# Performance work log

Measured on AMD Instinct MI355X. Metric: run time of the kernel, lower is better.

The kernel has to match this reference:

```python
import jax, jax.numpy as jnp
import numpy as np

L, BT, D = 1024, 64, 768
HID, NH, K = 192, 4, 5
T = 16
Hh = Ww = 32  # H = W = sqrt(L)


def setup_inputs() -> dict:
    key = jax.random.key(0)
    ks = jax.random.split(key, 10)
    s = 0.02
    def w(i, shape):
        return jax.random.normal(ks[i], shape, jnp.float32) * s
    return {
        "x": jax.random.normal(ks[0], (L, BT, D), jnp.float32),
        "fc1_w": w(1, (HID, D)), "fc1_b": jnp.zeros((HID,), jnp.float32),
        "convA_w": w(2, (64, HID)), "convA_b": jnp.zeros((64,), jnp.float32),
        "convB_w": w(3, (HID, 64)), "convB_b": jnp.zeros((HID,), jnp.float32),
        "ln_g": jnp.ones((HID,), jnp.float32), "ln_b": jnp.zeros((HID,), jnp.float32),
        "qkv_w": w(4, (3 * HID, HID)), "qkv_b": jnp.zeros((3 * HID,), jnp.float32),
        "rpb": w(5, (NH, 2 * K - 1, 2 * K - 1)),
        "proj_w": w(6, (HID, HID)), "proj_b": jnp.zeros((HID,), jnp.float32),
        "fc2_w": w(7, (D, HID)), "fc2_b": jnp.zeros((D,), jnp.float32),
    }


def _layernorm(x, g, b, eps=1e-5):
    # fp32 LayerNorm over last dim (matches the fp16-safe LayerNorm subclass)
    xf = x.astype(jnp.float32)
    m = xf.mean(-1, keepdims=True)
    v = ((xf - m) ** 2).mean(-1, keepdims=True)
    return ((xf - m) / jnp.sqrt(v + eps) * g + b).astype(x.dtype)


def _natten2d(x, qkv_w, qkv_b, rpb, proj_w, proj_b):
    # Neighborhood attention: each pixel attends to an edge-clamped KxK window.
    B, H, W, C = x.shape
    hd = C // NH
    qkv = (x @ qkv_w.T + qkv_b).reshape(B, H, W, 3, NH, hd)
    q, k, v = qkv[..., 0, :, :], qkv[..., 1, :, :], qkv[..., 2, :, :]
    q = q * (hd ** -0.5)
    half = K // 2
    ih = jnp.clip(jnp.arange(H) - half, 0, H - K)[:, None] + jnp.arange(K)  # [H,K]
    iw = jnp.clip(jnp.arange(W) - half, 0, W - K)[:, None] + jnp.arange(K)  # [W,K]
    k_nb = k[:, ih][:, :, :, iw]  # [B,H,K,W,K,NH,hd]
    v_nb = v[:, ih][:, :, :, iw]
    attn = jnp.einsum('bijnd,bixjynd->bnijxy', q, k_nb)  # [B,NH,H,W,K,K]
    bh = ih - jnp.arange(H)[:, None] + (K - 1)  # [H,K] in [0, 2K-2]
    bw = iw - jnp.arange(W)[:, None] + (K - 1)  # [W,K]
    bias = rpb[:, bh][:, :, :, bw]              # [NH,H,K,W,K]
    attn = attn + bias.transpose(0, 1, 3, 2, 4)[None]
    a = jax.nn.softmax(attn.reshape(B, NH, H, W, K * K), axis=-1)
    a = a.reshape(B, NH, H, W, K, K)
    out = jnp.einsum('bnijxy,bixjynd->bijnd', a, v_nb).reshape(B, H, W, C)
    return out @ proj_w.T + proj_b


def _forward(x, fc1_w, fc1_b, convA_w, convA_b, convB_w, convB_b,
             ln_g, ln_b, qkv_w, qkv_b, rpb, proj_w, proj_b, fc2_w, fc2_b):
    # x: [L, BT, D]
    xs = x @ fc1_w.T + fc1_b  # [L, BT, HID]
    # 1x1 Conv1d pair over the channel (HID) dim; dropout is identity in eval
    a = jnp.einsum('lbc,oc->lbo', xs, convA_w) + convA_b
    b_ = jnp.einsum('lbo,co->lbc', a, convB_w) + convB_b
    xs = b_ + xs  # scale = 1
    xs = jax.nn.gelu(xs, approximate=False)
    xs = xs.transpose(1, 0, 2).reshape(BT, Hh, Ww, HID)  # [BT,H,W,C]
    xs = xs + _natten2d(_layernorm(xs, ln_g, ln_b), qkv_w, qkv_b, rpb, proj_w, proj_b)
    xs = xs.reshape(BT, L, HID).transpose(1, 0, 2)  # [L,BT,HID]
    xs = xs @ fc2_w.T + fc2_b  # [L,BT,D]
    x = x + xs
    x = x.transpose(1, 0, 2).reshape(BT, Hh, Ww, D)
    x = x.reshape(BT // T, T, Hh, Ww, D).transpose(0, 4, 1, 2, 3)  # [B,D,T,H,W]
    return x


def reference(x, fc1_w, fc1_b, convA_w, convA_b, convB_w, convB_b,
              ln_g, ln_b, qkv_w, qkv_b, rpb, proj_w, proj_b, fc2_w, fc2_b):
    return _forward(x, fc1_w, fc1_b, convA_w, convA_b, convB_w, convB_b,
                    ln_g, ln_b, qkv_w, qkv_b, rpb, proj_w, proj_b, fc2_w, fc2_b)
```

## Files before the change

### kernel.cpp

```cpp
#include <hip/hip_runtime.h>
#include <hip/hip_bf16.h>
#include <math.h>


typedef __attribute__((ext_vector_type(4))) float f32x4;
typedef __attribute__((ext_vector_type(8))) __bf16 bf16x8;
typedef const __attribute__((address_space(1))) void gv_t;
typedef __attribute__((address_space(3))) void lv_t;

__device__ __forceinline__ uint2 pack_bf16x4(float4 v) {
  union { unsigned short u[4]; uint2 d; } o;
  __hip_bfloat16 b0 = __float2bfloat16(v.x);
  __hip_bfloat16 b1 = __float2bfloat16(v.y);
  __hip_bfloat16 b2 = __float2bfloat16(v.z);
  __hip_bfloat16 b3 = __float2bfloat16(v.w);
  o.u[0] = *(unsigned short*)&b0; o.u[1] = *(unsigned short*)&b1;
  o.u[2] = *(unsigned short*)&b2; o.u[3] = *(unsigned short*)&b3;
  return o.d;
}

__global__ __launch_bounds__(512, 4) void fc1_kernel(
    const float* __restrict__ X, const __hip_bfloat16* __restrict__ W,
    const float* __restrict__ bias, __hip_bfloat16* __restrict__ C) {
  __shared__ __hip_bfloat16 Asm[2][128 * 64];
  __shared__ __hip_bfloat16 Bsm[2][192 * 64];

  const int tid = threadIdx.x;
  const int lane = tid & 63;
  const int wave = tid >> 6;
  const int lid = blockIdx.x;
  const int bm0 = (((lid & 7) << 6) + (lid >> 3)) << 7;
  const int wm0 = (wave >> 1) * 32;
  const int wn0 = (wave & 1) * 96;
  const int l15 = lane & 15;
  const int l7 = lane & 7;
  const int lg = lane >> 4;

  f32x4 acc[2][6] = {};
  float4 ar[4];

  auto stageB = [&](int buf, int k0) {
#pragma unroll
    for (int it = 0; it < 3; ++it) {
      int ci = tid + it * 512;
      int r = ci >> 3, c = ci & 7;
      int sc = c ^ (r & 7);
      const __hip_bfloat16* src = W + (size_t)r * 768 + k0 + sc * 8;
      __builtin_amdgcn_global_load_lds((gv_t*)src, (lv_t*)&Bsm[buf][ci * 8], 16, 0, 0);
    }
  };
  auto loadA = [&](int k0) {
#pragma unroll
    for (int q = 0; q < 2; ++q) {
      int ci = tid + q * 512;
      int r = ci >> 3, c = ci & 7;
      int sc = c ^ (r & 7);
      const float* src = X + (size_t)(bm0 + r) * 768 + k0 + sc * 8;
      ar[2 * q] = *(const float4*)src;
      ar[2 * q + 1] = *(const float4*)(src + 4);
    }
  };
  auto writeA = [&](int buf) {
#pragma unroll
    for (int q = 0; q < 2; ++q) {
      int ci = tid + q * 512;
      uint2 a = pack_bf16x4(ar[2 * q]);
      uint2 b = pack_bf16x4(ar[2 * q + 1]);
      uint4 w; w.x = a.x; w.y = a.y; w.z = b.x; w.w = b.y;
      *(uint4*)&Asm[buf][ci * 8] = w;
    }
  };

  stageB(0, 0);
  loadA(0);
  int cur = 0;
  for (int kt = 0; kt < 12; ++kt) {
    writeA(cur);
    __syncthreads();
    if (kt < 11) { stageB(cur ^ 1, (kt + 1) * 64); loadA((kt + 1) * 64); }
    const char* Ab = (const char*)&Asm[cur][0];
    const char* Bb = (const char*)&Bsm[cur][0];
#pragma unroll
    for (int kk = 0; kk < 2; ++kk) {
      const int ks = (lg * 16 + kk * 64) ^ (l7 << 4);
      bf16x8 af[2], bfr[6];
#pragma unroll
      for (int mi = 0; mi < 2; ++mi)
        af[mi] = *(const bf16x8*)(Ab + (wm0 + mi * 16 + l15) * 128 + ks);
#pragma unroll
      for (int nj = 0; nj < 6; ++nj)
        bfr[nj] = *(const bf16x8*)(Bb + (wn0 + nj * 16 + l15) * 128 + ks);
#pragma unroll
      for (int mi = 0; mi < 2; ++mi)
#pragma unroll
        for (int nj = 0; nj < 6; ++nj)
          acc[mi][nj] = __builtin_amdgcn_mfma_f32_16x16x32_bf16(
              af[mi], bfr[nj], acc[mi][nj], 0, 0, 0);
    }
    cur ^= 1;
  }

#pragma unroll
  for (int nj = 0; nj < 6; ++nj) {
    const int n = wn0 + nj * 16 + l15;
    const float bi = bias[n];
#pragma unroll
    for (int mi = 0; mi < 2; ++mi) {
      const int mb = bm0 + wm0 + mi * 16 + lg * 4;
#pragma unroll
      for (int r = 0; r < 4; ++r)
        C[(size_t)(mb + r) * 192 + n] = __float2bfloat16(acc[mi][nj][r] + bi);
    }
  }
}

template <int MODE>
__global__ __launch_bounds__(256) void gemm_fullk_kernel(
    const __hip_bfloat16* __restrict__ A, const __hip_bfloat16* __restrict__ W,
    const float* __restrict__ bias, const __hip_bfloat16* __restrict__ res,
    const float* __restrict__ xin, void* __restrict__ Cout, int N) {
  __shared__ __hip_bfloat16 Asm[3 * 128 * 64];
  __shared__ __hip_bfloat16 Bsm[3 * 64 * 64];

  const int tid = threadIdx.x;
  const int lane = tid & 63;
  const int wave = tid >> 6;

  const int gx = gridDim.x;
  const int lid = blockIdx.y * gx + blockIdx.x;
  const int seq = lid >> 3;
  const int bm0 = (((lid & 7) << 6) + seq / gx) << 7;
  const int bn0 = (seq % gx) * 64;

  const int wm0 = (wave >> 1) * 64;
  const int wn0 = (wave & 1) * 32;
  const int l15 = lane & 15;
  const int l7 = lane & 7;
  const int lg = lane >> 4;

#pragma unroll
  for (int it = 0; it < 12; ++it) {
    int ci = tid + it * 256;
    int sec = ci >> 10, ri = ci & 1023;
    int r = ri >> 3, c = ri & 7;
    int sc = c ^ (r & 7);
    const __hip_bfloat16* src = A + (size_t)(bm0 + r) * 192 + sec * 64 + sc * 8;
    __builtin_amdgcn_global_load_lds((gv_t*)src, (lv_t*)&Asm[ci * 8], 16, 0, 0);
  }
#pragma unroll
  for (int it = 0; it < 6; ++it) {
    int ci = tid + it * 256;
    int sec = ci >> 9, ri = ci & 511;
    int r = ri >> 3, c = ri & 7;
    int sc = c ^ (r & 7);
    const __hip_bfloat16* src = W + (size_t)(bn0 + r) * 192 + sec * 64 + sc * 8;
    __builtin_amdgcn_global_load_lds((gv_t*)src, (lv_t*)&Bsm[ci * 8], 16, 0, 0);
  }
  __syncthreads();

  f32x4 acc[4][2] = {};
  const char* Ab = (const char*)Asm;
  const char* Bb = (const char*)Bsm;
#pragma unroll
  for (int kk = 0; kk < 6; ++kk) {
    const int sec = kk >> 1, k2 = kk & 1;
    const int ks = (lg * 16 + k2 * 64) ^ (l7 << 4);
    bf16x8 af[4], bfr[2];
#pragma unroll
    for (int mi = 0; mi < 4; ++mi)
      af[mi] = *(const bf16x8*)(Ab + sec * 16384 + (wm0 + mi * 16 + l15) * 128 + ks);
#pragma unroll
    for (int nj = 0; nj < 2; ++nj)
      bfr[nj] = *(const bf16x8*)(Bb + sec * 8192 + (wn0 + nj * 16 + l15) * 128 + ks);
#pragma unroll
    for (int mi = 0; mi < 4; ++mi)
#pragma unroll
      for (int nj = 0; nj < 2; ++nj) {
        if constexpr (MODE == 2)
          acc[mi][nj] = __builtin_amdgcn_mfma_f32_16x16x32_bf16(
              bfr[nj], af[mi], acc[mi][nj], 0, 0, 0);
        else
          acc[mi][nj] = __builtin_amdgcn_mfma_f32_16x16x32_bf16(
              af[mi], bfr[nj], acc[mi][nj], 0, 0, 0);
      }
  }

  if constexpr (MODE == 2) {
    float* Cf = (float*)Cout;
#pragma unroll
    for (int nj = 0; nj < 2; ++nj) {
      const int n0 = bn0 + wn0 + nj * 16 + lg * 4;
      const f32x4 bi4 = *(const f32x4*)(bias + n0);
#pragma unroll
      for (int mi = 0; mi < 4; ++mi) {
        const int m = bm0 + wm0 + mi * 16 + l15;
        const int b = m >> 10;
        const int ll = m & 1023;
        const f32x4 xv = *(const f32x4*)(xin + (size_t)((ll << 6) | b) * 768 + n0);
        const size_t ob = (((size_t)(b >> 4) * 768 + n0) * 16 + (b & 15)) * 1024 + ll;
#pragma unroll
        for (int r = 0; r < 4; ++r)
          Cf[ob + (size_t)r * 16384] = acc[mi][nj][r] + bi4[r] + xv[r];
      }
    }
  } else {
    __hip_bfloat16* Cb = (__hip_bfloat16*)Cout;
#pragma unroll
    for (int nj = 0; nj < 2; ++nj) {
      const int n = bn0 + wn0 + nj * 16 + l15;
      const float bi = bias[n];
#pragma unroll
      for (int mi = 0; mi < 4; ++mi) {
        const int mb = bm0 + wm0 + mi * 16 + lg * 4;
        f32x4 v = acc[mi][nj];
#pragma unroll
        for (int r = 0; r < 4; ++r) {
          const int m = mb + r;
          float val = v[r] + bi;
          if constexpr (MODE == 1) val += __bfloat162float(res[(size_t)m * N + n]);
          Cb[(size_t)m * N + n] = __float2bfloat16(val);
        }
      }
    }
  }
}

__global__ __launch_bounds__(256) void cvt_weights_kernel(
    const float* __restrict__ s0, const float* __restrict__ s1,
    const float* __restrict__ s2, const float* __restrict__ s3,
    const float* __restrict__ s4, const float* __restrict__ s5,
    __hip_bfloat16* __restrict__ d0, __hip_bfloat16* __restrict__ d1,
    __hip_bfloat16* __restrict__ d2, __hip_bfloat16* __restrict__ d3,
    __hip_bfloat16* __restrict__ d4, __hip_bfloat16* __restrict__ d5) {
  int i = blockIdx.x * 256 + threadIdx.x;
  const float* src; __hip_bfloat16* dst; int off;
  if      (i < 36864)  { src = s0; dst = d0; off = i; }
  else if (i < 39936)  { src = s1; dst = d1; off = i - 36864; }
  else if (i < 43008)  { src = s2; dst = d2; off = i - 39936; }
  else if (i < 70656)  { src = s3; dst = d3; off = i - 43008; }
  else if (i < 79872)  { src = s4; dst = d4; off = i - 70656; }
  else                 { src = s5; dst = d5; off = i - 79872; }
  ((uint2*)dst)[off] = pack_bf16x4(((const float4*)src)[off]);
}

__global__ __launch_bounds__(256, 2) void bottleneck_kernel(
    const __hip_bfloat16* __restrict__ xs0,
    const __hip_bfloat16* __restrict__ wA, const float* __restrict__ bA,
    const __hip_bfloat16* __restrict__ wB, const float* __restrict__ bB,
    const float* __restrict__ ln_g, const float* __restrict__ ln_b,
    __hip_bfloat16* __restrict__ xs_sp, __hip_bfloat16* __restrict__ ln_sp) {
  __shared__ __hip_bfloat16 xt[3 * 64 * 64];
  __shared__ __hip_bfloat16 wAs[3 * 64 * 64];
  __shared__ __hip_bfloat16 wBs[192 * 64];
  __shared__ __hip_bfloat16 a2[64 * 64];

  const int tid = threadIdx.x;
  const int lane = tid & 63;
  const int wave = tid >> 6;
  const int bm0 = blockIdx.x * 64;
  const int l15 = lane & 15;
  const int lg = lane >> 4;
  const int wm0 = (wave >> 1) * 32;

#pragma unroll
  for (int it = 0; it < 6; ++it) {
    int ci = tid + it * 256;
    int sec = ci >> 9, ri = ci & 511;
    int r = ri >> 3, c = ri & 7;
    int sc = c ^ (r & 7);
    const __hip_bfloat16* src = xs0 + (size_t)(bm0 + r) * 192 + sec * 64 + sc * 8;
    __builtin_amdgcn_global_load_lds((gv_t*)src, (lv_t*)&xt[ci * 8], 16, 0, 0);
  }
#pragma unroll
  for (int it = 0; it < 6; ++it) {
    int ci = tid + it * 256;
    int sec = ci >> 9, ri = ci & 511;
    int r = ri >> 3, c = ri & 7;
    int sc = c ^ (r & 7);
    const __hip_bfloat16* src = wA + (size_t)r * 192 + sec * 64 + sc * 8;
    __builtin_amdgcn_global_load_lds((gv_t*)src, (lv_t*)&wAs[ci * 8], 16, 0, 0);
  }
#pragma unroll
  for (int it = 0; it < 6; ++it) {
    int ci = tid + it * 256;
    int r = ci >> 3, c = ci & 7;
    int sc = c ^ (r & 7);
    const __hip_bfloat16* src = wB + (size_t)r * 64 + sc * 8;
    __builtin_amdgcn_global_load_lds((gv_t*)src, (lv_t*)&wBs[ci * 8], 16, 0, 0);
  }
  __syncthreads();

  {
    const int wn0 = (wave & 1) * 32;
    f32x4 acc1[2][2] = {};
    const char* Ab = (const char*)xt;
    const char* Bb = (const char*)wAs;
#pragma unroll
    for (int kk = 0; kk < 6; ++kk) {
      const int sec = kk >> 1, k2 = kk & 1;
      const int ks = (lg * 16 + k2 * 64) ^ ((l15 & 7) << 4);
      bf16x8 af[2], bfr[2];
#pragma unroll
      for (int mi = 0; mi < 2; ++mi)
        af[mi] = *(const bf16x8*)(Ab + sec * 8192 + (wm0 + mi * 16 + l15) * 128 + ks);
#pragma unroll
      for (int nj = 0; nj < 2; ++nj)
        bfr[nj] = *(const bf16x8*)(Bb + sec * 8192 + (wn0 + nj * 16 + l15) * 128 + ks);
#pragma unroll
      for (int mi = 0; mi < 2; ++mi)
#pragma unroll
        for (int nj = 0; nj < 2; ++nj)
          acc1[mi][nj] = __builtin_amdgcn_mfma_f32_16x16x32_bf16(
              af[mi], bfr[nj], acc1[mi][nj], 0, 0, 0);
    }
#pragma unroll
    for (int nj = 0; nj < 2; ++nj) {
      const int n = wn0 + nj * 16 + l15;
      const float bi = bA[n];
#pragma unroll
      for (int mi = 0; mi < 2; ++mi)
#pragma unroll
        for (int r = 0; r < 4; ++r) {
          const int row = wm0 + mi * 16 + lg * 4 + r;
          a2[row * 64 + (((n >> 3) ^ (row & 7)) << 3) + (n & 7)] =
              __float2bfloat16(acc1[mi][nj][r] + bi);
        }
    }
  }
  __syncthreads();

  const int wn0 = (wave & 1) * 96;
  f32x4 acc2[2][6] = {};
  {
    const char* Ab = (const char*)a2;
    const char* Bb = (const char*)wBs;
#pragma unroll
    for (int kk = 0; kk < 2; ++kk) {
      const int ks = (lg * 16 + kk * 64) ^ ((l15 & 7) << 4);
      bf16x8 af[2], bfr[6];
#pragma unroll
      for (int mi = 0; mi < 2; ++mi)
        af[mi] = *(const bf16x8*)(Ab + (wm0 + mi * 16 + l15) * 128 + ks);
#pragma unroll
      for (int nj = 0; nj < 6; ++nj)
        bfr[nj] = *(const bf16x8*)(Bb + (wn0 + nj * 16 + l15) * 128 + ks);
#pragma unroll
      for (int mi = 0; mi < 2; ++mi)
#pragma unroll
        for (int nj = 0; nj < 6; ++nj)
          acc2[mi][nj] = __builtin_amdgcn_mfma_f32_16x16x32_bf16(
              af[mi], bfr[nj], acc2[mi][nj], 0, 0, 0);
    }
  }
  __syncthreads();

  float* stats = (float*)a2;

#pragma unroll
  for (int nj = 0; nj < 6; ++nj) {
    const int n = wn0 + nj * 16 + l15;
    const float bi = bB[n];
    const int sec = n >> 6, n6 = n & 63;
#pragma unroll
    for (int mi = 0; mi < 2; ++mi)
#pragma unroll
      for (int r = 0; r < 4; ++r) {
        const int row = wm0 + mi * 16 + lg * 4 + r;
        const int ei = sec * 4096 + row * 64 + (((n6 >> 3) ^ (row & 7)) << 3) + (n6 & 7);
        float v = acc2[mi][nj][r] + bi + __bfloat162float(xt[ei]);
        float ge = 0.5f * v * (1.0f + erff(v * 0.70710678118654752f));
        acc2[mi][nj][r] = ge;
        xt[ei] = __float2bfloat16(ge);
      }
  }
#pragma unroll
  for (int mi = 0; mi < 2; ++mi)
#pragma unroll
    for (int r = 0; r < 4; ++r) {
      float s1 = 0.0f, s2 = 0.0f;
#pragma unroll
      for (int nj = 0; nj < 6; ++nj) {
        float v = acc2[mi][nj][r];
        s1 += v;
        s2 += v * v;
      }
#pragma unroll
      for (int off = 1; off < 16; off <<= 1) {
        s1 += __shfl_xor(s1, off);
        s2 += __shfl_xor(s2, off);
      }
      if (l15 == 0) {
        const int row = wm0 + mi * 16 + lg * 4 + r;
        stats[row * 4 + (wave & 1) * 2 + 0] = s1;
        stats[row * 4 + (wave & 1) * 2 + 1] = s2;
      }
    }
  __syncthreads();

#pragma unroll
  for (int it = 0; it < 6; ++it) {
    int ci = tid + it * 256;
    int row = ci / 24, gr = ci % 24;
    int sec = gr >> 3, g8i = gr & 7;
    bf16x8 g8 = *(const bf16x8*)&xt[sec * 4096 + row * 64 + ((g8i ^ (row & 7)) << 3)];
    float s1 = stats[row * 4 + 0] + stats[row * 4 + 2];
    float s2 = stats[row * 4 + 1] + stats[row * 4 + 3];
    float mean = s1 * (1.0f / 192.0f);
    float var = s2 * (1.0f / 192.0f) - mean * mean;
    float rstd = rsqrtf(var + 1e-5f);
    const int m_l = bm0 + row;
    const size_t dst = ((size_t)(((m_l & 63) << 10) | (m_l >> 6))) * 192 + gr * 8;
    bf16x8 lnv;
#pragma unroll
    for (int u = 0; u < 8; ++u) {
      float g = (float)g8[u];
      lnv[u] = (__bf16)((g - mean) * rstd * ln_g[gr * 8 + u] + ln_b[gr * 8 + u]);
    }
    *(bf16x8*)(xs_sp + dst) = g8;
    *(bf16x8*)(ln_sp + dst) = lnv;
  }
}

__global__ __launch_bounds__(256) void natten_kernel(
    const __hip_bfloat16* __restrict__ qkv, const float* __restrict__ rpb,
    __hip_bfloat16* __restrict__ o) {
  __shared__ __hip_bfloat16 kv_s[2816 * 8];
  __shared__ __hip_bfloat16 q_s[1536 * 8];

  const int tid = threadIdx.x;
  const int bid = blockIdx.x;
  const int head = bid & 3;
  const int tj = (bid >> 2) & 1;
  const int ti = (bid >> 3) & 1;
  const int b = bid >> 4;

  const int hs = ti * 12;
  const int ws = tj * 12;
  const int i = ti * 16 + (tid >> 4);
  const int j = tj * 16 + (tid & 15);
  const int pix = (b << 10) + (i << 5) + j;
  const int ih0 = min(max(i - 2, 0), 27);
  const int iw0 = min(max(j - 2, 0), 27);
  const int oi = ih0 - hs;
  const int oj = iw0 - ws;
  const int dbh = ih0 - i + 4;
  const int dbw = iw0 - j + 4;
  const size_t kbase = (size_t)(b << 10) * 576 + 192 + head * 48;

#pragma unroll
  for (int it = 0; it < 6; ++it) {
    int ci = tid + it * 256;
    int px = ci / 6, c = ci % 6;
    int pi = ti * 16 + (px >> 4), pj = tj * 16 + (px & 15);
    const __hip_bfloat16* src =
        qkv + (size_t)((b << 10) + (pi << 5) + pj) * 576 + head * 48 + c * 8;
    __builtin_amdgcn_global_load_lds((gv_t*)src, (lv_t*)&q_s[ci * 8], 16, 0, 0);
  }
#pragma unroll
  for (int it = 0; it < 11; ++it) {
    int ci = tid + it * 256;
    int r = ci / 7, c = ci % 7;
    int hr = r / 20, wr = r % 20;
    const __hip_bfloat16* src =
        qkv + kbase + (size_t)((hs + hr) * 32 + (ws + wr)) * 576 + c * 8;
    __builtin_amdgcn_global_load_lds((gv_t*)src, (lv_t*)&kv_s[ci * 8], 16, 0, 0);
  }

  float s[25];
#pragma unroll
  for (int x = 0; x < 5; ++x)
#pragma unroll
    for (int y = 0; y < 5; ++y)
      s[x * 5 + y] = rpb[head * 81 + (dbh + x) * 9 + (dbw + y)] * 6.9282032302755092f;

  __syncthreads();

  const char* qb = (const char*)q_s + tid * 96;
  const char* kvb = (const char*)kv_s + (oi * 20 + oj) * 112;
#pragma unroll
  for (int t = 0; t < 6; ++t) {
    const bf16x8 qv = *(const bf16x8*)(qb + t * 16);
#pragma unroll
    for (int x = 0; x < 5; ++x) {
#pragma unroll
      for (int y = 0; y < 5; ++y) {
        const bf16x8 kv = *(const bf16x8*)(kvb + (x * 20 + y) * 112 + t * 16);
        float a = 0.0f;
#pragma unroll
        for (int u = 0; u < 8; ++u) a += (float)qv[u] * (float)kv[u];
        s[x * 5 + y] += a;
      }
    }
  }
  __syncthreads();

#pragma unroll
  for (int it = 0; it < 11; ++it) {
    int ci = tid + it * 256;
    int r = ci / 7, c = ci % 7;
    int hr = r / 20, wr = r % 20;
    const __hip_bfloat16* src =
        qkv + kbase + 192 + (size_t)((hs + hr) * 32 + (ws + wr)) * 576 + c * 8;
    __builtin_amdgcn_global_load_lds((gv_t*)src, (lv_t*)&kv_s[ci * 8], 16, 0, 0);
  }

  float mx = s[0];
#pragma unroll
  for (int n = 1; n < 25; ++n) mx = fmaxf(mx, s[n]);
  float sum = 0.0f;
#pragma unroll
  for (int n = 0; n < 25; ++n) {
    s[n] = __expf((s[n] - mx) * 0.14433756729740643f);
    sum += s[n];
  }
  const float inv = 1.0f / sum;

  __syncthreads();

  bf16x8* op = (bf16x8*)(o + (size_t)pix * 192 + head * 48);
#pragma unroll
  for (int t = 0; t < 6; ++t) {
    float pv[8] = {};
#pragma unroll
    for (int x = 0; x < 5; ++x) {
#pragma unroll
      for (int y = 0; y < 5; ++y) {
        const bf16x8 vv = *(const bf16x8*)(kvb + (x * 20 + y) * 112 + t * 16);
        const float w = s[x * 5 + y];
#pragma unroll
        for (int u = 0; u < 8; ++u) pv[u] += w * (float)vv[u];
      }
    }
    bf16x8 ov;
#pragma unroll
    for (int u = 0; u < 8; ++u) ov[u] = (__bf16)(pv[u] * inv);
    op[t] = ov;
  }
}

extern "C" void kernel_launch(void* const* d_in, const int* in_sizes, int n_in,
                              void* d_out, int out_size, void* d_ws, size_t ws_size,
                              hipStream_t stream) {
  const float* x       = (const float*)d_in[0];
  const float* fc1_w   = (const float*)d_in[1];
  const float* fc1_b   = (const float*)d_in[2];
  const float* convA_w = (const float*)d_in[3];
  const float* convA_b = (const float*)d_in[4];
  const float* convB_w = (const float*)d_in[5];
  const float* convB_b = (const float*)d_in[6];
  const float* ln_g    = (const float*)d_in[7];
  const float* ln_b    = (const float*)d_in[8];
  const float* qkv_w   = (const float*)d_in[9];
  const float* qkv_b   = (const float*)d_in[10];
  const float* rpb     = (const float*)d_in[11];
  const float* proj_w  = (const float*)d_in[12];
  const float* proj_b  = (const float*)d_in[13];
  const float* fc2_w   = (const float*)d_in[14];
  const float* fc2_b   = (const float*)d_in[15];
  float* out = (float*)d_out;

  char* W0 = (char*)d_ws;
  __hip_bfloat16* wfc1  = (__hip_bfloat16*)W0;
  __hip_bfloat16* wcvA  = wfc1 + 147456;
  __hip_bfloat16* wcvB  = wcvA + 12288;
  __hip_bfloat16* wqkv  = wcvB + 12288;
  __hip_bfloat16* wproj = wqkv + 110592;
  __hip_bfloat16* wfc2  = wproj + 36864;
  __hip_bfloat16* reg1  = wfc2 + 147456;
  __hip_bfloat16* xs0   = reg1;
  __hip_bfloat16* qkvb  = reg1;
  __hip_bfloat16* ybuf  = reg1;
  __hip_bfloat16* xs_sp = reg1 + 37748736;
  __hip_bfloat16* ln_sp = xs_sp + 12582912;
  __hip_bfloat16* obuf  = ln_sp;

  cvt_weights_kernel<<<456, 256, 0, stream>>>(
      fc1_w, convA_w, convB_w, qkv_w, proj_w, fc2_w,
      wfc1, wcvA, wcvB, wqkv, wproj, wfc2);

  fc1_kernel<<<512, 512, 0, stream>>>(x, wfc1, fc1_b, xs0);
  bottleneck_kernel<<<1024, 256, 0, stream>>>(
      xs0, wcvA, convA_b, wcvB, convB_b, ln_g, ln_b, xs_sp, ln_sp);
  gemm_fullk_kernel<0><<<dim3(9, 512), 256, 0, stream>>>(
      ln_sp, wqkv, qkv_b, nullptr, nullptr, qkvb, 576);
  natten_kernel<<<1024, 256, 0, stream>>>(qkvb, rpb, obuf);
  gemm_fullk_kernel<1><<<dim3(3, 512), 256, 0, stream>>>(
      obuf, wproj, proj_b, xs_sp, nullptr, ybuf, 192);
  gemm_fullk_kernel<2><<<dim3(12, 512), 256, 0, stream>>>(
      ybuf, wfc2, fc2_b, nullptr, x, (void*)out, 768);
}
```

Measured before the change: 309.7 us.

## Store QKV in per-head planar layout and load Q directly into registers

The QKV GEMM epilogue (MODE 0) now writes q/k/v per head into separate contiguous planes of [pixels, 48]. The natten kernel then reads K/V tiles from contiguous 96-byte rows instead of strided 576-element rows, and loads Q straight into registers, which drops the Q shared-memory buffer. Launch bounds request 3 blocks per CU to raise occupancy. The scattered epilogue stores of individual bf16 values may be less coalesced, and the larger register footprint could cause spills.

```diff
diff --git a/kernel.cpp b/kernel.cpp
--- a/kernel.cpp
+++ b/kernel.cpp
@@ -7,6 +7,8 @@
 typedef __attribute__((ext_vector_type(8))) __bf16 bf16x8;
 typedef const __attribute__((address_space(1))) void gv_t;
 typedef __attribute__((address_space(3))) void lv_t;
+
+#define PLANE 3145728
 
 __device__ __forceinline__ uint2 pack_bf16x4(float4 v) {
   union { unsigned short u[4]; uint2 d; } o;
@@ -203,6 +205,26 @@
           Cf[ob + (size_t)r * 16384] = acc[mi][nj][r] + bi4[r] + xv[r];
       }
     }
+  } else if constexpr (MODE == 0) {
+    __hip_bfloat16* Cb = (__hip_bfloat16*)Cout;
+#pragma unroll
+    for (int nj = 0; nj < 2; ++nj) {
+      const int n = bn0 + wn0 + nj * 16 + l15;
+      const int p = n / 192;
+      const int rem = n - p * 192;
+      const int h = rem / 48;
+      const int d = rem - h * 48;
+      const size_t plane = (size_t)(p * 4 + h) * PLANE;
+      const float bi = bias[n];
+#pragma unroll
+      for (int mi = 0; mi < 4; ++mi) {
+        const int mb = bm0 + wm0 + mi * 16 + lg * 4;
+#pragma unroll
+        for (int r = 0; r < 4; ++r)
+          Cb[plane + (size_t)(mb + r) * 48 + d] =
+              __float2bfloat16(acc[mi][nj][r] + bi);
+      }
+    }
   } else {
     __hip_bfloat16* Cb = (__hip_bfloat16*)Cout;
 #pragma unroll
@@ -216,8 +238,7 @@
 #pragma unroll
         for (int r = 0; r < 4; ++r) {
           const int m = mb + r;
-          float val = v[r] + bi;
-          if constexpr (MODE == 1) val += __bfloat162float(res[(size_t)m * N + n]);
+          float val = v[r] + bi + __bfloat162float(res[(size_t)m * N + n]);
           Cb[(size_t)m * N + n] = __float2bfloat16(val);
         }
       }
@@ -421,11 +442,10 @@
   }
 }
 
-__global__ __launch_bounds__(256) void natten_kernel(
+__global__ __launch_bounds__(256, 3) void natten_kernel(
     const __hip_bfloat16* __restrict__ qkv, const float* __restrict__ rpb,
     __hip_bfloat16* __restrict__ o) {
   __shared__ __hip_bfloat16 kv_s[2816 * 8];
-  __shared__ __hip_bfloat16 q_s[1536 * 8];
 
   const int tid = threadIdx.x;
   const int bid = blockIdx.x;
@@ -445,25 +465,25 @@
   const int oj = iw0 - ws;
   const int dbh = ih0 - i + 4;
   const int dbw = iw0 - j + 4;
-  const size_t kbase = (size_t)(b << 10) * 576 + 192 + head * 48;
-
-#pragma unroll
-  for (int it = 0; it < 6; ++it) {
-    int ci = tid + it * 256;
-    int px = ci / 6, c = ci % 6;
-    int pi = ti * 16 + (px >> 4), pj = tj * 16 + (px & 15);
-    const __hip_bfloat16* src =
-        qkv + (size_t)((b << 10) + (pi << 5) + pj) * 576 + head * 48 + c * 8;
-    __builtin_amdgcn_global_load_lds((gv_t*)src, (lv_t*)&q_s[ci * 8], 16, 0, 0);
-  }
+
+  const __hip_bfloat16* Kp = qkv + (size_t)(4 + head) * PLANE;
+  const __hip_bfloat16* Vp = qkv + (size_t)(8 + head) * PLANE;
+
 #pragma unroll
   for (int it = 0; it < 11; ++it) {
     int ci = tid + it * 256;
     int r = ci / 7, c = ci % 7;
     int hr = r / 20, wr = r % 20;
     const __hip_bfloat16* src =
-        qkv + kbase + (size_t)((hs + hr) * 32 + (ws + wr)) * 576 + c * 8;
+        Kp + (size_t)((b << 10) + (hs + hr) * 32 + (ws + wr)) * 48 + c * 8;
     __builtin_amdgcn_global_load_lds((gv_t*)src, (lv_t*)&kv_s[ci * 8], 16, 0, 0);
+  }
+
+  bf16x8 qv[6];
+  {
+    const bf16x8* qg = (const bf16x8*)(qkv + (size_t)head * PLANE + (size_t)pix * 48);
+#pragma unroll
+    for (int t = 0; t < 6; ++t) qv[t] = qg[t];
   }
 
   float s[25];
@@ -475,11 +495,10 @@
 
   __syncthreads();
 
-  const char* qb = (const char*)q_s + tid * 96;
   const char* kvb = (const char*)kv_s + (oi * 20 + oj) * 112;
 #pragma unroll
   for (int t = 0; t < 6; ++t) {
-    const bf16x8 qv = *(const bf16x8*)(qb + t * 16);
+    const bf16x8 q8 = qv[t];
 #pragma unroll
     for (int x = 0; x < 5; ++x) {
 #pragma unroll
@@ -487,7 +506,7 @@
         const bf16x8 kv = *(const bf16x8*)(kvb + (x * 20 + y) * 112 + t * 16);
         float a = 0.0f;
 #pragma unroll
-        for (int u = 0; u < 8; ++u) a += (float)qv[u] * (float)kv[u];
+        for (int u = 0; u < 8; ++u) a += (float)q8[u] * (float)kv[u];
         s[x * 5 + y] += a;
       }
     }
@@ -500,7 +519,7 @@
     int r = ci / 7, c = ci % 7;
     int hr = r / 20, wr = r % 20;
     const __hip_bfloat16* src =
-        qkv + kbase + 192 + (size_t)((hs + hr) * 32 + (ws + wr)) * 576 + c * 8;
+        Vp + (size_t)((b << 10) + (hs + hr) * 32 + (ws + wr)) * 48 + c * 8;
     __builtin_amdgcn_global_load_lds((gv_t*)src, (lv_t*)&kv_s[ci * 8], 16, 0, 0);
   }
 
```

Measured after the change: 489.9 us. +58.2%, slower.
